# Kernel tuning notes

Hardware: AMD Instinct MI355X
Metric: run time of the kernel (lower is better)

Reference implementation:

```python
import jax, jax.numpy as jnp
import numpy as np

B, N, L, D = 1, 128, 256, 256   # batch, num_seqs, seq_len, msa_dim
P, H = 128, 8                   # pair_dim, num_heads
DH = D // H                     # head_dim


def setup_inputs() -> dict:
    key = jax.random.key(0)
    ks = jax.random.split(key, 7)
    msa = jax.random.normal(ks[0], (B, N, L, D), dtype=jnp.float32)
    pair = jax.random.normal(ks[1], (B, L, L, P), dtype=jnp.float32)
    mask = jax.random.randint(ks[2], (B, N, L), 0, 2) > 0  # bool key mask
    w_qkv = jax.random.normal(ks[3], (D, 3 * D), dtype=jnp.float32) * (D ** -0.5)
    w_pb = jax.random.normal(ks[4], (P, H), dtype=jnp.float32) * (P ** -0.5)
    b_pb = jnp.zeros((H,), dtype=jnp.float32)
    w_out = jax.random.normal(ks[5], (D, D), dtype=jnp.float32) * (D ** -0.5)
    b_out = jnp.zeros((D,), dtype=jnp.float32)
    return {"msa": msa, "pair": pair, "mask": mask, "w_qkv": w_qkv,
            "w_pb": w_pb, "b_pb": b_pb, "w_out": w_out, "b_out": b_out}


def reference(msa, pair, mask, w_qkv, w_pb, b_pb, w_out, b_out):
    b, n, l, d = msa.shape
    scaling = DH ** -0.5
    qkv = msa @ w_qkv                                   # [b,n,l,3d]
    qkv = qkv.reshape(b, n, l, 3, H, DH)
    q, k, v = qkv[..., 0, :, :], qkv[..., 1, :, :], qkv[..., 2, :, :]  # [b,n,l,h,dh]
    pair_bias = (pair @ w_pb + b_pb)                    # [b,l,l,h]
    pair_bias = jnp.transpose(pair_bias, (0, 3, 1, 2))  # [b,h,l,l]
    # scores: [b,n,h,l,l]
    dots = jnp.einsum('bnqhd,bnkhd->bnhqk', q, k) * scaling
    dots = dots + pair_bias[:, None]                    # broadcast over num_seqs
    dots = jnp.where(mask[:, :, None, None, :], dots, -jnp.inf)  # mask keys
    attn = jax.nn.softmax(dots, axis=-1)
    out = jnp.einsum('bnhqk,bnkhd->bnqhd', attn, v)     # [b,n,l,h,dh]
    out = out.reshape(b, n, l, d)
    return out @ w_out + b_out
```

## Files before the change

### kernel.cpp

```cpp
#include <hip/hip_runtime.h>
#include <hip/hip_bf16.h>

#define NN 128
#define LL 256
#define DD 256
#define PP 128
#define HH 8
#define DHH 32

typedef __bf16 bf16x8 __attribute__((ext_vector_type(8)));
typedef short s16x4 __attribute__((ext_vector_type(4)));
typedef short s16x8 __attribute__((ext_vector_type(8)));
typedef float f32x4 __attribute__((ext_vector_type(4)));
typedef unsigned int u32x2 __attribute__((ext_vector_type(2)));

__device__ __forceinline__ int permk(int k) {
  return (k & 0xC3) | ((k & 0x30) >> 2) | ((k & 0x0C) << 2);
}

__device__ __forceinline__ void gload_lds16(const void* g, void* l) {
  __builtin_amdgcn_global_load_lds(
      (const __attribute__((address_space(1))) void*)g,
      (__attribute__((address_space(3))) void*)l, 16, 0, 0);
}

__global__ __launch_bounds__(256) void cvt_bf16(
    const float* __restrict__ src, __hip_bfloat16* __restrict__ dst, int n) {
  for (int i = (blockIdx.x * 256 + threadIdx.x) * 4; i < n; i += gridDim.x * 1024) {
    float4 v = *(const float4*)(src + i);
    ushort4 o;
    o.x = __bfloat16_as_ushort(__float2bfloat16(v.x));
    o.y = __bfloat16_as_ushort(__float2bfloat16(v.y));
    o.z = __bfloat16_as_ushort(__float2bfloat16(v.z));
    o.w = __bfloat16_as_ushort(__float2bfloat16(v.w));
    *(ushort4*)(dst + i) = o;
  }
}

__global__ __launch_bounds__(256) void transpose_cvt(
    const float* __restrict__ src, __hip_bfloat16* __restrict__ dst,
    int K, int N) {
  __shared__ float t[32][33];
  int n0 = blockIdx.x * 32, k0 = blockIdx.y * 32;
  int tx = threadIdx.x & 31, ty = threadIdx.x >> 5;
  for (int i = 0; i < 4; ++i) {
    int ky = ty + i * 8;
    t[ky][tx] = src[(size_t)(k0 + ky) * N + n0 + tx];
  }
  __syncthreads();
  for (int i = 0; i < 4; ++i) {
    int ny = ty + i * 8;
    dst[(size_t)(n0 + ny) * K + k0 + tx] = __float2bfloat16(t[tx][ny]);
  }
}

#define MODE_I32 0
#define MODE_I8 1
#define MODE_BF16 2
#define MODE_F32 3

__global__ __launch_bounds__(256) void mask_expand(
    const unsigned char* __restrict__ mraw, float* __restrict__ mout) {
  __shared__ int s_or1, s_or2, s_or3, s_max, s_mode;
  int tid = threadIdx.x;
  if (tid == 0) { s_or1 = 0; s_or2 = 0; s_or3 = 0; s_max = 0; }
  __syncthreads();
  int or1 = 0, or2 = 0, or3 = 0, mx = 0;
  for (int j = tid; j < 4096; j += 256) {
    int b = mraw[j];
    mx = mx > b ? mx : b;
    int r = j & 3;
    if (r == 1) or1 |= b;
    else if (r == 2) or2 |= b;
    else if (r == 3) or3 |= b;
  }
  atomicOr(&s_or1, or1); atomicOr(&s_or2, or2); atomicOr(&s_or3, or3);
  atomicMax(&s_max, mx);
  __syncthreads();
  if (tid == 0) {
    int mode;
    if (s_max <= 1) mode = ((s_or1 | s_or2 | s_or3) == 0) ? MODE_I32 : MODE_I8;
    else            mode = (s_or1 != 0) ? MODE_BF16 : MODE_F32;
    s_mode = mode;
  }
  __syncthreads();
  int mode = s_mode;
  int i0 = blockIdx.x * 1024;
  for (int i = i0 + tid; i < i0 + 1024; i += 256) {
    int v;
    if (mode == MODE_I32)       v = ((const int*)mraw)[i] != 0;
    else if (mode == MODE_I8)   v = mraw[i] != 0;
    else if (mode == MODE_BF16) v = ((const unsigned short*)mraw)[i] != 0;
    else                        v = ((const unsigned int*)mraw)[i] != 0;
    mout[(i & ~255) | permk(i & 255)] = v ? 1.f : 0.f;
  }
}

#define GEMM_MAINLOOP(Aptr, Btptr)                                            \
  __shared__ __align__(16) __hip_bfloat16 Asm[128 * 32];                      \
  __shared__ __align__(16) __hip_bfloat16 Bsm[128 * 32];                      \
  int tid = threadIdx.x;                                                      \
  int lane = tid & 63;                                                        \
  int wv = tid >> 6;                                                          \
  int wm = (wv >> 1) * 64, wn = (wv & 1) * 64;                                \
  int lr = lane & 15, quad = lane >> 4;                                       \
  int bm = blockIdx.x, bn = blockIdx.y;                                       \
  f32x4 acc[4][4];                                                            \
  for (int i = 0; i < 4; ++i)                                                 \
    for (int j = 0; j < 4; ++j) acc[i][j] = (f32x4){0.f, 0.f, 0.f, 0.f};      \
  for (int ks = 0; ks < 8; ++ks) {                                            \
    int k0 = ks * 32;                                                         \
    if (ks) __syncthreads();                                                  \
    for (int i = 0; i < 2; ++i) {                                             \
      int c = tid + i * 256;                                                  \
      int row = c >> 2, cc = c & 3;                                           \
      int ldsbase = (wv * 64 + i * 256) * 8;      \
      gload_lds16(Aptr + ((size_t)(bm * 128 + row)) * 256 + k0 + cc * 8,      \
                  Asm + ldsbase);                                             \
      gload_lds16(Btptr + ((size_t)(bn * 128 + row)) * 256 + k0 + cc * 8,     \
                  Bsm + ldsbase);                                             \
    }                                                                         \
    __syncthreads();                                                          \
    bf16x8 af[4], bfr[4];                                                     \
    for (int mi = 0; mi < 4; ++mi)                                            \
      af[mi] = *(const bf16x8*)&Asm[(wm + mi * 16 + lr) * 32 + quad * 8];     \
    for (int ni = 0; ni < 4; ++ni)                                            \
      bfr[ni] = *(const bf16x8*)&Bsm[(wn + ni * 16 + lr) * 32 + quad * 8];    \
    for (int mi = 0; mi < 4; ++mi)                                            \
      for (int ni = 0; ni < 4; ++ni)                                          \
        acc[mi][ni] = __builtin_amdgcn_mfma_f32_16x16x32_bf16(                \
            af[mi], bfr[ni], acc[mi][ni], 0, 0, 0);                           \
  }

__global__ __launch_bounds__(256) void qkv_gemm_mfma(
    const __hip_bfloat16* __restrict__ A,
    const __hip_bfloat16* __restrict__ Bt,
    __hip_bfloat16* __restrict__ qb,
    __hip_bfloat16* __restrict__ kb,
    __hip_bfloat16* __restrict__ vb) {
  GEMM_MAINLOOP(A, Bt)
  for (int mi = 0; mi < 4; ++mi) {
    for (int ni = 0; ni < 4; ++ni) {
      int gcol = bn * 128 + wn + ni * 16 + lr;
      int t = gcol >> 8, rem = gcol & 255;
      int h = rem >> 5, dh = rem & 31;
      for (int r = 0; r < 4; ++r) {
        int grow = bm * 128 + wm + mi * 16 + quad * 4 + r;
        int n = grow >> 8, l = grow & 255;
        __hip_bfloat16 val = __float2bfloat16(acc[mi][ni][r]);
        if (t == 0)
          qb[(size_t)(((n * HH + h) * LL + l)) * DHH + dh] = val;
        else if (t == 1)
          kb[(size_t)(((n * HH + h) * LL + l)) * DHH + dh] = val;
        else
          vb[(size_t)(((n * HH + h) * DHH + dh)) * LL + permk(l)] = val;
      }
    }
  }
}

__global__ __launch_bounds__(256) void out_gemm_mfma(
    const __hip_bfloat16* __restrict__ A,
    const __hip_bfloat16* __restrict__ Bt,
    const float* __restrict__ bout,
    float* __restrict__ C) {
  GEMM_MAINLOOP(A, Bt)
  for (int mi = 0; mi < 4; ++mi) {
    for (int ni = 0; ni < 4; ++ni) {
      int gcol = bn * 128 + wn + ni * 16 + lr;
      float bo = bout[gcol];
      for (int r = 0; r < 4; ++r) {
        int grow = bm * 128 + wm + mi * 16 + quad * 4 + r;
        C[(size_t)grow * 256 + gcol] = acc[mi][ni][r] + bo;
      }
    }
  }
}

__global__ __launch_bounds__(256) void pair_bias_kernel(
    const float* __restrict__ pair,
    const float* __restrict__ w_pb,
    const float* __restrict__ b_pb,
    __hip_bfloat16* __restrict__ expb) {
  __shared__ float wp[128][9];
  __shared__ float rows[32][129];
  int tid = threadIdx.x;
  for (int i = 0; i < 4; ++i) {
    int e = tid + i * 256;
    wp[e >> 3][e & 7] = w_pb[e];
  }
  int row0 = blockIdx.x * 32;
  const float* src = pair + (size_t)row0 * PP;
  for (int i = 0; i < 16; ++i) {
    int e = tid + i * 256;
    int r = e >> 7, c = e & 127;
    rows[r][c] = src[r * 128 + c];
  }
  __syncthreads();
  int h = tid >> 5, rl = tid & 31;
  float acc = b_pb[h] - 12.0f;
  for (int p = 0; p < 128; ++p)
    acc += rows[rl][p] * wp[p][h];
  int row = row0 + rl;
  int i = row >> 8, j = row & 255;
  expb[((size_t)(h * LL + i)) * LL + permk(j)] = __float2bfloat16(__expf(acc));
}

__global__ __launch_bounds__(256, 2) void attn_mfma(
    const __hip_bfloat16* __restrict__ qb,
    const __hip_bfloat16* __restrict__ kb,
    const __hip_bfloat16* __restrict__ vbt,
    const __hip_bfloat16* __restrict__ expb,
    const float* __restrict__ maskf,
    __hip_bfloat16* __restrict__ ao) {
  int bx = blockIdx.x;
  int h = bx >> 7, n = bx & 127;
  int nh = n * HH + h;
  int tid = threadIdx.x, lane = tid & 63, wv = tid >> 6;
  int lr = lane & 15, quad = lane >> 4;
  int wm = wv * 64;
  size_t base = (size_t)nh * (LL * DHH);

  const __hip_bfloat16* qp = qb + base;
  const __hip_bfloat16* kp = kb + base;
  const __hip_bfloat16* vp = vbt + base;
  const __hip_bfloat16* ep = expb + (size_t)h * LL * LL;
  const float* mrow = maskf + n * LL;

  const float cs = 0.17677669529663687f * 1.4426950408889634f;

  bf16x8 aq[4];
#pragma unroll
  for (int mi = 0; mi < 4; ++mi)
    aq[mi] = *(const bf16x8*)(qp + (size_t)(wm + mi * 16 + lr) * DHH + quad * 8);

  bf16x8 bkA[4], bkB[4];
  s16x8 avA0a, avA0b, avA1a, avA1b;
  s16x8 avB0a, avB0b, avB1a, avB1b;
  uint4 e0a, e0b, e1a, e1b, e2a, e2b, e3a, e3b;
  f32x4 mw0, mw1, mw2, mw3;

#define LOADKT(S, KT)                                                          \
  {                                                                            \
    const int j0_ = (KT) * 64;                                                 \
    _Pragma("unroll") for (int nj = 0; nj < 4; ++nj)                           \
        bk##S[nj] =                                                            \
        *(const bf16x8*)(kp + (size_t)(j0_ + nj * 16 + lr) * DHH + quad * 8);  \
    av##S##0a = *(const s16x8*)(vp + (size_t)lr * LL + j0_ + quad * 16);       \
    av##S##0b = *(const s16x8*)(vp + (size_t)lr * LL + j0_ + quad * 16 + 8);   \
    av##S##1a = *(const s16x8*)(vp + (size_t)(16 + lr) * LL + j0_ + quad * 16);\
    av##S##1b =                                                                \
        *(const s16x8*)(vp + (size_t)(16 + lr) * LL + j0_ + quad * 16 + 8);    \
  }

#define LOADEB_ALL(KT)                                                         \
  {                                                                            \
    const int j0_ = (KT) * 64;                                                 \
    e0a = *(const uint4*)(ep + (size_t)(wm + 0 + lr) * LL + j0_ + quad * 16);  \
    e0b = *(const uint4*)(ep + (size_t)(wm + 0 + lr) * LL + j0_ + quad * 16 + 8);\
    e1a = *(const uint4*)(ep + (size_t)(wm + 16 + lr) * LL + j0_ + quad * 16); \
    e1b = *(const uint4*)(ep + (size_t)(wm + 16 + lr) * LL + j0_ + quad * 16 + 8);\
    e2a = *(const uint4*)(ep + (size_t)(wm + 32 + lr) * LL + j0_ + quad * 16); \
    e2b = *(const uint4*)(ep + (size_t)(wm + 32 + lr) * LL + j0_ + quad * 16 + 8);\
    e3a = *(const uint4*)(ep + (size_t)(wm + 48 + lr) * LL + j0_ + quad * 16); \
    e3b = *(const uint4*)(ep + (size_t)(wm + 48 + lr) * LL + j0_ + quad * 16 + 8);\
  }

#define LOADMW(KT)                                                             \
  {                                                                            \
    const int j0_ = (KT) * 64;                                                 \
    mw0 = *(const f32x4*)(mrow + j0_ + quad * 16 + 0);                         \
    mw1 = *(const f32x4*)(mrow + j0_ + quad * 16 + 4);                         \
    mw2 = *(const f32x4*)(mrow + j0_ + quad * 16 + 8);                         \
    mw3 = *(const f32x4*)(mrow + j0_ + quad * 16 + 12);                        \
  }

#define NJ_STEP(C, MI, NJ, EX, EY, AV0, AV1, LO)                               \
  {                                                                            \
    f32x4 s_ = __builtin_amdgcn_mfma_f32_16x16x32_bf16(                        \
        bk##C[NJ], aq[MI], (f32x4){0.f, 0.f, 0.f, 0.f}, 0, 0, 0);              \
    float em0_ = __uint_as_float((EX) << 16) * mw##NJ[0];                      \
    float em1_ = __uint_as_float((EX) & 0xffff0000u) * mw##NJ[1];              \
    float em2_ = __uint_as_float((EY) << 16) * mw##NJ[2];                      \
    float em3_ = __uint_as_float((EY) & 0xffff0000u) * mw##NJ[3];              \
    float p0_ = exp2f(s_[0] * cs) * em0_;                                      \
    float p1_ = exp2f(s_[1] * cs) * em1_;                                      \
    float p2_ = exp2f(s_[2] * cs) * em2_;                                      \
    float p3_ = exp2f(s_[3] * cs) * em3_;                                      \
    lsum[MI] += (p0_ + p1_) + (p2_ + p3_);                                     \
    unsigned lo_ =                                                             \
        ((unsigned)__bfloat16_as_ushort(__float2bfloat16(p1_)) << 16) |        \
        (unsigned)__bfloat16_as_ushort(__float2bfloat16(p0_));                 \
    unsigned hi_ =                                                             \
        ((unsigned)__bfloat16_as_ushort(__float2bfloat16(p3_)) << 16) |        \
        (unsigned)__bfloat16_as_ushort(__float2bfloat16(p2_));                 \
    u32x2 pu_ = {lo_, hi_};                                                    \
    s16x4 pb_ = __builtin_bit_cast(s16x4, pu_);                                \
    s16x4 a0_ = __builtin_shufflevector(AV0, AV0, LO, LO + 1, LO + 2, LO + 3); \
    s16x4 a1_ = __builtin_shufflevector(AV1, AV1, LO, LO + 1, LO + 2, LO + 3); \
    o_acc[MI][0] = __builtin_amdgcn_mfma_f32_16x16x16bf16_1k(                  \
        a0_, pb_, o_acc[MI][0], 0, 0, 0);                                      \
    o_acc[MI][1] = __builtin_amdgcn_mfma_f32_16x16x16bf16_1k(                  \
        a1_, pb_, o_acc[MI][1], 0, 0, 0);                                      \
  }

#define MI_PHASE(MI, C, EA, EB_)                                               \
  {                                                                            \
    NJ_STEP(C, MI, 0, EA.x, EA.y, av##C##0a, av##C##1a, 0)                     \
    NJ_STEP(C, MI, 1, EA.z, EA.w, av##C##0a, av##C##1a, 4)                     \
    NJ_STEP(C, MI, 2, EB_.x, EB_.y, av##C##0b, av##C##1b, 0)                   \
    NJ_STEP(C, MI, 3, EB_.z, EB_.w, av##C##0b, av##C##1b, 4)                   \
  }

#define KT_PHASE(KT, C, N, LAST)                                               \
  {                                                                            \
    LOADEB_ALL(KT)                                                             \
    LOADMW(KT)                                                                 \
    if (!(LAST)) LOADKT(N, (KT) + 1)                                           \
    MI_PHASE(0, C, e0a, e0b)                                                   \
    MI_PHASE(1, C, e1a, e1b)                                                   \
    MI_PHASE(2, C, e2a, e2b)                                                   \
    MI_PHASE(3, C, e3a, e3b)                                                   \
  }

  float lsum[4] = {0.f, 0.f, 0.f, 0.f};
  f32x4 o_acc[4][2];
#pragma unroll
  for (int mi = 0; mi < 4; ++mi)
#pragma unroll
    for (int no = 0; no < 2; ++no) o_acc[mi][no] = (f32x4){0.f, 0.f, 0.f, 0.f};

  LOADKT(A, 0)

  KT_PHASE(0, A, B, 0)
  KT_PHASE(1, B, A, 0)
  KT_PHASE(2, A, B, 0)
  KT_PHASE(3, B, A, 1)

#undef LOADKT
#undef LOADEB_ALL
#undef LOADMW
#undef NJ_STEP
#undef MI_PHASE
#undef KT_PHASE

#pragma unroll
  for (int mi = 0; mi < 4; ++mi) {
    float ls = lsum[mi];
    ls += __shfl_xor(ls, 16);
    ls += __shfl_xor(ls, 32);
    float inv = (ls > 0.f) ? 1.f / ls : 0.f;
    int q = wm + mi * 16 + lr;
#pragma unroll
    for (int no = 0; no < 2; ++no) {
      f32x4 o = o_acc[mi][no];
      ushort4 w;
      w.x = __bfloat16_as_ushort(__float2bfloat16(o[0] * inv));
      w.y = __bfloat16_as_ushort(__float2bfloat16(o[1] * inv));
      w.z = __bfloat16_as_ushort(__float2bfloat16(o[2] * inv));
      w.w = __bfloat16_as_ushort(__float2bfloat16(o[3] * inv));
      *(ushort4*)(ao + (size_t)n * (LL * DD) + (size_t)q * DD +
                  h * DHH + no * 16 + quad * 4) = w;
    }
  }
}

extern "C" void kernel_launch(void* const* d_in, const int* in_sizes, int n_in,
                              void* d_out, int out_size, void* d_ws, size_t ws_size,
                              hipStream_t stream) {
  const float* msa   = (const float*)d_in[0];
  const float* pair  = (const float*)d_in[1];
  const unsigned char* mask = (const unsigned char*)d_in[2];
  const float* w_qkv = (const float*)d_in[3];
  const float* w_pb  = (const float*)d_in[4];
  const float* b_pb  = (const float*)d_in[5];
  const float* w_out = (const float*)d_in[6];
  const float* b_out = (const float*)d_in[7];
  float* out = (float*)d_out;

  char* ws = (char*)d_ws;
  __hip_bfloat16* qb      = (__hip_bfloat16*)(ws);
  __hip_bfloat16* kb      = (__hip_bfloat16*)(ws + 16777216);
  __hip_bfloat16* vb      = (__hip_bfloat16*)(ws + 33554432);
  __hip_bfloat16* msa_c   = (__hip_bfloat16*)(ws + 50331648);
  __hip_bfloat16* ao      = (__hip_bfloat16*)(ws + 50331648);
  __hip_bfloat16* expb    = (__hip_bfloat16*)(ws + 67108864);
  __hip_bfloat16* wqkv_t  = (__hip_bfloat16*)(ws + 71303168);
  __hip_bfloat16* wout_t  = (__hip_bfloat16*)(ws + 71696384);
  float*          msk     = (float*)(ws + 71827456);

  mask_expand<<<32, 256, 0, stream>>>(mask, msk);
  cvt_bf16<<<1024, 256, 0, stream>>>(msa, msa_c, NN * LL * DD);
  transpose_cvt<<<dim3(24, 8), 256, 0, stream>>>(w_qkv, wqkv_t, 256, 768);
  transpose_cvt<<<dim3(8, 8), 256, 0, stream>>>(w_out, wout_t, 256, 256);

  qkv_gemm_mfma<<<dim3(256, 6), 256, 0, stream>>>(msa_c, wqkv_t, qb, kb, vb);
  pair_bias_kernel<<<2048, 256, 0, stream>>>(pair, w_pb, b_pb, expb);
  attn_mfma<<<1024, 256, 0, stream>>>(qb, kb, vb, expb, msk, ao);
  out_gemm_mfma<<<dim3(256, 2), 256, 0, stream>>>(ao, wout_t, b_out, out);
}
```

Baseline: 241.7 us.

## Double-buffer GEMM LDS tiles, swizzle LDS layout, vectorize epilogue stores

Rewrites the shared GEMM main loop used by the QKV and output projections to double-buffer the A/B tiles in LDS. The next k-slice's global-to-LDS loads are issued before the current slice's MFMAs, and the loop is fully unrolled with one barrier per step. It also XOR-swizzles the LDS column slot to cut bank conflicts. Swapping the MFMA operands transposes the accumulator fragment so the epilogues can write 4 contiguous outputs per lane: ushort4 for q/k and float4 plus bias for the output GEMM. This doubles LDS use per block, which may lower occupancy.

```diff
diff --git a/kernel.cpp b/kernel.cpp
--- a/kernel.cpp
+++ b/kernel.cpp
@@ -96,41 +96,63 @@
   }
 }
 
-#define GEMM_MAINLOOP(Aptr, Btptr)                                            \
-  __shared__ __align__(16) __hip_bfloat16 Asm[128 * 32];                      \
-  __shared__ __align__(16) __hip_bfloat16 Bsm[128 * 32];                      \
+#define GSTAGE(AD, BD, KS)                                                    \
+  {                                                                           \
+    const int k0_ = (KS) * 32;                                                \
+    gload_lds16(Aptr + ((size_t)(bm * 128 + srow)) * 256 + k0_ + scc * 8,     \
+                AD + (size_t)(wv * 64) * 8);                                  \
+    gload_lds16(Btptr + ((size_t)(bn * 128 + srow)) * 256 + k0_ + scc * 8,    \
+                BD + (size_t)(wv * 64) * 8);                                  \
+    gload_lds16(Aptr + ((size_t)(bm * 128 + 64 + srow)) * 256 + k0_ + scc * 8,\
+                AD + (size_t)(wv * 64 + 256) * 8);                            \
+    gload_lds16(Btptr + ((size_t)(bn * 128 + 64 + srow)) * 256 + k0_ + scc * 8,\
+                BD + (size_t)(wv * 64 + 256) * 8);                            \
+  }
+
+#define GPHASE(CA, CB, NA, NB, NKS, DOSTAGE)                                  \
+  {                                                                           \
+    if (DOSTAGE) GSTAGE(NA, NB, NKS)                                          \
+    bf16x8 af[4], bfr[4];                                                     \
+    _Pragma("unroll") for (int mi = 0; mi < 4; ++mi) {                        \
+      int r_ = wm + mi * 16 + lr;                                             \
+      af[mi] = *(const bf16x8*)&CA[r_ * 32 + (quad ^ (r_ & 3)) * 8];          \
+    }                                                                         \
+    _Pragma("unroll") for (int ni = 0; ni < 4; ++ni) {                        \
+      int r_ = wn + ni * 16 + lr;                                             \
+      bfr[ni] = *(const bf16x8*)&CB[r_ * 32 + (quad ^ (r_ & 3)) * 8];         \
+    }                                                                         \
+    _Pragma("unroll") for (int mi = 0; mi < 4; ++mi)                          \
+      _Pragma("unroll") for (int ni = 0; ni < 4; ++ni)                        \
+        acc[mi][ni] = __builtin_amdgcn_mfma_f32_16x16x32_bf16(                \
+            bfr[ni], af[mi], acc[mi][ni], 0, 0, 0);                           \
+  }                                                                           \
+  __syncthreads();
+
+#define GEMM_PIPELINE(APTR_, BTPTR_)                                          \
+  const __hip_bfloat16* __restrict__ Aptr = (APTR_);                          \
+  const __hip_bfloat16* __restrict__ Btptr = (BTPTR_);                        \
+  __shared__ __align__(16) __hip_bfloat16 As0[128 * 32], As1[128 * 32];       \
+  __shared__ __align__(16) __hip_bfloat16 Bs0[128 * 32], Bs1[128 * 32];       \
   int tid = threadIdx.x;                                                      \
-  int lane = tid & 63;                                                        \
-  int wv = tid >> 6;                                                          \
+  int lane = tid & 63, wv = tid >> 6;                                         \
   int wm = (wv >> 1) * 64, wn = (wv & 1) * 64;                                \
   int lr = lane & 15, quad = lane >> 4;                                       \
   int bm = blockIdx.x, bn = blockIdx.y;                                       \
+  int srow = tid >> 2, sslot = tid & 3;                                       \
+  int scc = sslot ^ (srow & 3);                                               \
   f32x4 acc[4][4];                                                            \
   for (int i = 0; i < 4; ++i)                                                 \
     for (int j = 0; j < 4; ++j) acc[i][j] = (f32x4){0.f, 0.f, 0.f, 0.f};      \
-  for (int ks = 0; ks < 8; ++ks) {                                            \
-    int k0 = ks * 32;                                                         \
-    if (ks) __syncthreads();                                                  \
-    for (int i = 0; i < 2; ++i) {                                             \
-      int c = tid + i * 256;                                                  \
-      int row = c >> 2, cc = c & 3;                                           \
-      int ldsbase = (wv * 64 + i * 256) * 8;      \
-      gload_lds16(Aptr + ((size_t)(bm * 128 + row)) * 256 + k0 + cc * 8,      \
-                  Asm + ldsbase);                                             \
-      gload_lds16(Btptr + ((size_t)(bn * 128 + row)) * 256 + k0 + cc * 8,     \
-                  Bsm + ldsbase);                                             \
-    }                                                                         \
-    __syncthreads();                                                          \
-    bf16x8 af[4], bfr[4];                                                     \
-    for (int mi = 0; mi < 4; ++mi)                                            \
-      af[mi] = *(const bf16x8*)&Asm[(wm + mi * 16 + lr) * 32 + quad * 8];     \
-    for (int ni = 0; ni < 4; ++ni)                                            \
-      bfr[ni] = *(const bf16x8*)&Bsm[(wn + ni * 16 + lr) * 32 + quad * 8];    \
-    for (int mi = 0; mi < 4; ++mi)                                            \
-      for (int ni = 0; ni < 4; ++ni)                                          \
-        acc[mi][ni] = __builtin_amdgcn_mfma_f32_16x16x32_bf16(                \
-            af[mi], bfr[ni], acc[mi][ni], 0, 0, 0);                           \
-  }
+  GSTAGE(As0, Bs0, 0)                                                         \
+  __syncthreads();                                                            \
+  GPHASE(As0, Bs0, As1, Bs1, 1, 1)                                            \
+  GPHASE(As1, Bs1, As0, Bs0, 2, 1)                                            \
+  GPHASE(As0, Bs0, As1, Bs1, 3, 1)                                            \
+  GPHASE(As1, Bs1, As0, Bs0, 4, 1)                                            \
+  GPHASE(As0, Bs0, As1, Bs1, 5, 1)                                            \
+  GPHASE(As1, Bs1, As0, Bs0, 6, 1)                                            \
+  GPHASE(As0, Bs0, As1, Bs1, 7, 1)                                            \
+  GPHASE(As1, Bs1, As0, Bs0, 8, 0)
 
 __global__ __launch_bounds__(256) void qkv_gemm_mfma(
     const __hip_bfloat16* __restrict__ A,
@@ -138,22 +160,30 @@
     __hip_bfloat16* __restrict__ qb,
     __hip_bfloat16* __restrict__ kb,
     __hip_bfloat16* __restrict__ vb) {
-  GEMM_MAINLOOP(A, Bt)
+  GEMM_PIPELINE(A, Bt)
+  int t = bn >> 1;
+#pragma unroll
   for (int mi = 0; mi < 4; ++mi) {
+    int g = bm * 128 + wm + mi * 16 + lr;
+    int n = g >> 8, l = g & 255;
+    int lp = permk(l);
+#pragma unroll
     for (int ni = 0; ni < 4; ++ni) {
-      int gcol = bn * 128 + wn + ni * 16 + lr;
-      int t = gcol >> 8, rem = gcol & 255;
-      int h = rem >> 5, dh = rem & 31;
-      for (int r = 0; r < 4; ++r) {
-        int grow = bm * 128 + wm + mi * 16 + quad * 4 + r;
-        int n = grow >> 8, l = grow & 255;
-        __hip_bfloat16 val = __float2bfloat16(acc[mi][ni][r]);
-        if (t == 0)
-          qb[(size_t)(((n * HH + h) * LL + l)) * DHH + dh] = val;
-        else if (t == 1)
-          kb[(size_t)(((n * HH + h) * LL + l)) * DHH + dh] = val;
-        else
-          vb[(size_t)(((n * HH + h) * DHH + dh)) * LL + permk(l)] = val;
+      int rem = (bn * 128 + wn + ni * 16 + quad * 4) & 255;
+      int h = rem >> 5, dh0 = rem & 31;
+      if (t < 2) {
+        ushort4 w;
+        w.x = __bfloat16_as_ushort(__float2bfloat16(acc[mi][ni][0]));
+        w.y = __bfloat16_as_ushort(__float2bfloat16(acc[mi][ni][1]));
+        w.z = __bfloat16_as_ushort(__float2bfloat16(acc[mi][ni][2]));
+        w.w = __bfloat16_as_ushort(__float2bfloat16(acc[mi][ni][3]));
+        __hip_bfloat16* dst = (t == 0 ? qb : kb);
+        *(ushort4*)(dst + ((size_t)((n * HH + h) * LL + l)) * DHH + dh0) = w;
+      } else {
+#pragma unroll
+        for (int r = 0; r < 4; ++r)
+          vb[((size_t)((n * HH + h) * DHH + dh0 + r)) * LL + lp] =
+              __float2bfloat16(acc[mi][ni][r]);
       }
     }
   }
@@ -164,15 +194,20 @@
     const __hip_bfloat16* __restrict__ Bt,
     const float* __restrict__ bout,
     float* __restrict__ C) {
-  GEMM_MAINLOOP(A, Bt)
+  GEMM_PIPELINE(A, Bt)
+#pragma unroll
   for (int mi = 0; mi < 4; ++mi) {
+    int g = bm * 128 + wm + mi * 16 + lr;
+#pragma unroll
     for (int ni = 0; ni < 4; ++ni) {
-      int gcol = bn * 128 + wn + ni * 16 + lr;
-      float bo = bout[gcol];
-      for (int r = 0; r < 4; ++r) {
-        int grow = bm * 128 + wm + mi * 16 + quad * 4 + r;
-        C[(size_t)grow * 256 + gcol] = acc[mi][ni][r] + bo;
-      }
+      int gcol0 = bn * 128 + wn + ni * 16 + quad * 4;
+      float4 bo = *(const float4*)(bout + gcol0);
+      float4 v;
+      v.x = acc[mi][ni][0] + bo.x;
+      v.y = acc[mi][ni][1] + bo.y;
+      v.z = acc[mi][ni][2] + bo.z;
+      v.w = acc[mi][ni][3] + bo.w;
+      *(float4*)(C + (size_t)g * 256 + gcol0) = v;
     }
   }
 }
```

After: 224.5 us. 1.08x faster.
